# Kernel tuning notes

Measured on AMD Instinct MI355X. Metric: run time of the kernel, lower is better.

## Reference

```python
import jax, jax.numpy as jnp
import numpy as np

N, E, D = 50000, 500000, 128   # nodes, edges, input feature dim
H, F = 4, 32                    # num_heads, features_per_head (H*F == MLP output 128)


def _layer_norm(x, scale, bias, eps=1e-6):
    mu = jnp.mean(x, axis=-1, keepdims=True)
    var = jnp.var(x, axis=-1, keepdims=True)
    return (x - mu) * jax.lax.rsqrt(var + eps) * scale + bias


def setup_inputs() -> dict:
    key = jax.random.key(0)
    ks = jax.random.split(key, 6)
    s = lambda fan_in: 1.0 / np.sqrt(fan_in)
    return {
        "nodes": jax.random.normal(ks[0], (N, D), jnp.float32),
        "W1": jax.random.normal(ks[1], (D, 128), jnp.float32) * s(D),
        "b1": jnp.zeros((128,), jnp.float32),
        "ln1_scale": jnp.ones((128,), jnp.float32),
        "ln1_bias": jnp.zeros((128,), jnp.float32),
        "W2": jax.random.normal(ks[2], (128, H * F), jnp.float32) * s(128),
        "b2": jnp.zeros((H * F,), jnp.float32),
        "ln2_scale": jnp.ones((H * F,), jnp.float32),
        "ln2_bias": jnp.zeros((H * F,), jnp.float32),
        "senders": jax.random.randint(ks[3], (E,), 0, N, dtype=jnp.int32),
        "receivers": jax.random.randint(ks[4], (E,), 0, N, dtype=jnp.int32),
    }


def reference(nodes, W1, b1, ln1_scale, ln1_bias, W2, b2, ln2_scale, ln2_bias,
              senders, receivers):
    # attention_query MLP (MLPTorso: Dense -> LayerNorm -> relu, activate_final=True)
    h = jnp.maximum(_layer_norm(nodes @ W1 + b1, ln1_scale, ln1_bias), 0.0)
    h = jnp.maximum(_layer_norm(h @ W2 + b2, ln2_scale, ln2_bias), 0.0)
    q = h.reshape(N, H, F)                       # [N, H, F]

    # gather per-edge sender/receiver projections (same math as per-edge MLP)
    sent = q[senders]                            # [E, H, F]
    recv = q[receivers]                          # [E, H, F]

    # per-edge, per-head attention logits
    logits = jnp.einsum('ehf,ehf->eh', sent, recv) / jnp.sqrt(jnp.float32(F))

    # segment softmax over incoming edges of each receiver node (jraph semantics)
    seg_max = jax.ops.segment_max(logits, receivers, num_segments=N)
    seg_max = jnp.where(jnp.isfinite(seg_max), seg_max, 0.0)  # empty segments
    unnorm = jnp.exp(logits - seg_max[receivers])
    denom = jax.ops.segment_sum(unnorm, receivers, num_segments=N)
    weights = unnorm / denom[receivers]          # [E, H]

    # weighted messages, scatter-sum to receiver nodes
    messages = sent * weights[..., None]         # [E, H, F]
    agg = jax.ops.segment_sum(messages, receivers, num_segments=N)  # [N, H, F]

    # node update: activation then average over heads (avg_multi_head=True)
    out = jnp.maximum(agg, 0.0)
    return jnp.mean(out, axis=1)                 # [N, F]
```

## Files before the change

### kernel.cpp

```cpp
#include <hip/hip_runtime.h>

constexpr int D  = 128;
constexpr int NH = 4;
constexpr int NF = 32;

typedef __attribute__((ext_vector_type(8))) short bfrag;
typedef __attribute__((ext_vector_type(4))) float ffrag;

__device__ __forceinline__ unsigned short bf16h(float x) {
    unsigned u = __float_as_uint(x);
    u += 0x7fffu + ((u >> 16) & 1u);
    return (unsigned short)(u >> 16);
}
__device__ __forceinline__ float bf16tof(unsigned short h) {
    return __uint_as_float(((unsigned)h) << 16);
}

__global__ __launch_bounds__(256) void zero_cnt_kernel(int* __restrict__ p, int n)
{
    const int i4 = (blockIdx.x * blockDim.x + threadIdx.x) * 4;
    if (i4 + 3 < n) {
        *(int4*)&p[i4] = {0, 0, 0, 0};
    } else if (i4 < n) {
        for (int i = i4; i < n; ++i) p[i] = 0;
    }
}

__global__ __launch_bounds__(256) void wsplit_kernel(
    const float* __restrict__ W1, const float* __restrict__ W2,
    unsigned short* __restrict__ wt)
{
    const int L  = blockIdx.x >> 3;
    const int ct = blockIdx.x & 7;
    const float* W = L ? W2 : W1;
    const int ks   = threadIdx.x >> 6;
    const int lane = threadIdx.x & 63;
    const int lg = lane >> 4, lc = lane & 15;
    unsigned short* Hp = wt + ((size_t)(L * 2 + 0) * 32 + ct * 4 + ks) * 512 + lane * 8;
    unsigned short* Lp = wt + ((size_t)(L * 2 + 1) * 32 + ct * 4 + ks) * 512 + lane * 8;
    #pragma unroll
    for (int i = 0; i < 8; ++i) {
        const int k = ks * 32 + lg * 8 + i;
        const int c = ct * 16 + lc;
        const float v = W[(size_t)k * 128 + c];
        const unsigned short hh = bf16h(v);
        Hp[i] = hh;
        Lp[i] = bf16h(v - bf16tof(hh));
    }
}

__global__ __launch_bounds__(256, 2) void mlp_pipe_kernel(
    const float* __restrict__ X,
    const unsigned short* __restrict__ WF,
    const float* __restrict__ b1, const float* __restrict__ g1, const float* __restrict__ be1,
    const float* __restrict__ b2, const float* __restrict__ g2, const float* __restrict__ be2,
    unsigned short* __restrict__ Q, int N)
{
    constexpr int PW = 132;
    __shared__ unsigned HL[4 * 16 * PW];

    const int tid  = threadIdx.x;
    const int lane = tid & 63;
    const int wave = tid >> 6;
    const int lc   = lane & 15;
    const int lg   = lane >> 4;
    const int n0w  = (blockIdx.x * 4 + wave) * 16;
    if (n0w >= N) return;
    unsigned* hl = &HL[wave * 16 * PW];

    bfrag ah[4], al[4];

    {
        const int rowx = (n0w + lc < N) ? (n0w + lc) : (N - 1);
        const float* xr = X + (size_t)rowx * 128 + lg * 8;
        #pragma unroll
        for (int ks = 0; ks < 4; ++ks) {
            const float4 a = *(const float4*)&xr[ks * 32];
            const float4 b = *(const float4*)&xr[ks * 32 + 4];
            const float f[8] = {a.x, a.y, a.z, a.w, b.x, b.y, b.z, b.w};
            #pragma unroll
            for (int i = 0; i < 8; ++i) {
                const unsigned short hh = bf16h(f[i]);
                ah[ks][i] = (short)hh;
                al[ks][i] = (short)bf16h(f[i] - bf16tof(hh));
            }
        }
    }

    bfrag Bh0[4], Bl0[4], Bh1[4], Bl1[4];
    ffrag accF[8];

#define LOADB(BH, BL, hiBase, loBase, ctg)                                     \
    {                                                                          \
        const unsigned short* hp_ = WF + (size_t)((hiBase) + (ctg) * 4) * 512 + lane * 8; \
        const unsigned short* lp_ = WF + (size_t)((loBase) + (ctg) * 4) * 512 + lane * 8; \
        _Pragma("unroll")                                                      \
        for (int ks_ = 0; ks_ < 4; ++ks_) {                                    \
            BH[ks_] = *(const bfrag*)(hp_ + ks_ * 512);                        \
            BL[ks_] = *(const bfrag*)(lp_ + ks_ * 512);                        \
        }                                                                      \
    }

#define COMPB(BH, BL, dst)                                                     \
    {                                                                          \
        ffrag aH_ = (ffrag){0.f, 0.f, 0.f, 0.f};                               \
        ffrag aX_ = (ffrag){0.f, 0.f, 0.f, 0.f};                               \
        _Pragma("unroll")                                                      \
        for (int ks_ = 0; ks_ < 4; ++ks_) {                                    \
            aH_ = __builtin_amdgcn_mfma_f32_16x16x32_bf16(ah[ks_], BH[ks_], aH_, 0, 0, 0); \
            aX_ = __builtin_amdgcn_mfma_f32_16x16x32_bf16(ah[ks_], BL[ks_], aX_, 0, 0, 0); \
            aX_ = __builtin_amdgcn_mfma_f32_16x16x32_bf16(al[ks_], BH[ks_], aX_, 0, 0, 0); \
        }                                                                      \
        dst = aH_ + aX_;                                                       \
    }

#define GEMM_LAYER(hiBase, loBase)                                             \
    LOADB(Bh0, Bl0, hiBase, loBase, 0)                                         \
    LOADB(Bh1, Bl1, hiBase, loBase, 1)                                         \
    __builtin_amdgcn_sched_barrier(0);                                         \
    COMPB(Bh0, Bl0, accF[0])                                                   \
    LOADB(Bh0, Bl0, hiBase, loBase, 2)                                         \
    __builtin_amdgcn_sched_barrier(0);                                         \
    COMPB(Bh1, Bl1, accF[1])                                                   \
    LOADB(Bh1, Bl1, hiBase, loBase, 3)                                         \
    __builtin_amdgcn_sched_barrier(0);                                         \
    COMPB(Bh0, Bl0, accF[2])                                                   \
    LOADB(Bh0, Bl0, hiBase, loBase, 4)                                         \
    __builtin_amdgcn_sched_barrier(0);                                         \
    COMPB(Bh1, Bl1, accF[3])                                                   \
    LOADB(Bh1, Bl1, hiBase, loBase, 5)                                         \
    __builtin_amdgcn_sched_barrier(0);                                         \
    COMPB(Bh0, Bl0, accF[4])                                                   \
    LOADB(Bh0, Bl0, hiBase, loBase, 6)                                         \
    __builtin_amdgcn_sched_barrier(0);                                         \
    COMPB(Bh1, Bl1, accF[5])                                                   \
    LOADB(Bh1, Bl1, hiBase, loBase, 7)                                         \
    __builtin_amdgcn_sched_barrier(0);                                         \
    COMPB(Bh0, Bl0, accF[6])                                                   \
    COMPB(Bh1, Bl1, accF[7])

    GEMM_LAYER(0, 32)

    {
        float bb[8], gg[8], tt[8];
        #pragma unroll
        for (int ct = 0; ct < 8; ++ct) {
            const int col = ct * 16 + lc;
            bb[ct] = b1[col]; gg[ct] = g1[col]; tt[ct] = be1[col];
        }
        #pragma unroll
        for (int j = 0; j < 4; ++j) {
            float t[8], s = 0.f, ss = 0.f;
            #pragma unroll
            for (int ct = 0; ct < 8; ++ct) {
                t[ct] = accF[ct][j] + bb[ct];
                s += t[ct]; ss += t[ct] * t[ct];
            }
            #pragma unroll
            for (int off = 1; off <= 8; off <<= 1) {
                s  += __shfl_xor(s,  off, 16);
                ss += __shfl_xor(ss, off, 16);
            }
            const float mu   = s * (1.f / 128.f);
            const float var  = fmaxf(ss * (1.f / 128.f) - mu * mu, 0.f);
            const float rstd = rsqrtf(var + 1e-6f);
            const int row = lg * 4 + j;
            #pragma unroll
            for (int ct = 0; ct < 8; ++ct) {
                const float o = fmaxf((t[ct] - mu) * rstd * gg[ct] + tt[ct], 0.f);
                const unsigned short hh = bf16h(o);
                const unsigned short ll = bf16h(o - bf16tof(hh));
                hl[row * PW + ct * 16 + lc] = (unsigned)hh | ((unsigned)ll << 16);
            }
        }
    }

    asm volatile("s_waitcnt lgkmcnt(0)" ::: "memory");

    #pragma unroll
    for (int ks = 0; ks < 4; ++ks) {
        const uint4 r0 = *(const uint4*)&hl[lc * PW + ks * 32 + lg * 8];
        const uint4 r1 = *(const uint4*)&hl[lc * PW + ks * 32 + lg * 8 + 4];
        const unsigned rr[8] = {r0.x, r0.y, r0.z, r0.w, r1.x, r1.y, r1.z, r1.w};
        #pragma unroll
        for (int i = 0; i < 8; ++i) {
            ah[ks][i] = (short)(rr[i] & 0xffffu);
            al[ks][i] = (short)(rr[i] >> 16);
        }
    }

    GEMM_LAYER(64, 96)

#undef GEMM_LAYER
#undef COMPB
#undef LOADB

    {
        float bb[8], gg[8], tt[8];
        #pragma unroll
        for (int ct = 0; ct < 8; ++ct) {
            const int col = ct * 16 + lc;
            bb[ct] = b2[col]; gg[ct] = g2[col]; tt[ct] = be2[col];
        }
        #pragma unroll
        for (int j = 0; j < 4; ++j) {
            float t[8], s = 0.f, ss = 0.f;
            #pragma unroll
            for (int ct = 0; ct < 8; ++ct) {
                t[ct] = accF[ct][j] + bb[ct];
                s += t[ct]; ss += t[ct] * t[ct];
            }
            #pragma unroll
            for (int off = 1; off <= 8; off <<= 1) {
                s  += __shfl_xor(s,  off, 16);
                ss += __shfl_xor(ss, off, 16);
            }
            const float mu   = s * (1.f / 128.f);
            const float var  = fmaxf(ss * (1.f / 128.f) - mu * mu, 0.f);
            const float rstd = rsqrtf(var + 1e-6f);
            const int grow = n0w + lg * 4 + j;
            if (grow < N) {
                #pragma unroll
                for (int ct = 0; ct < 8; ++ct) {
                    const float o = fmaxf((t[ct] - mu) * rstd * gg[ct] + tt[ct], 0.f);
                    Q[(size_t)grow * 128 + ct * 16 + lc] = bf16h(o);
                }
            }
        }
    }
}

__global__ __launch_bounds__(256) void hist_kernel(
    const int* __restrict__ recv, int* __restrict__ cnt, int E)
{
    int i = blockIdx.x * blockDim.x + threadIdx.x;
    if (i < E) atomicAdd(&cnt[recv[i]], 1);
}

__global__ __launch_bounds__(256) void scan_blocks_kernel(
    const int* __restrict__ cnt, int* __restrict__ rowptr,
    int* __restrict__ bsum, int N)
{
    __shared__ int lds[256];
    const int tid = threadIdx.x;
    const int base = blockIdx.x * 1024 + tid * 4;
    int v0 = (base + 0 < N) ? cnt[base + 0] : 0;
    int v1 = (base + 1 < N) ? cnt[base + 1] : 0;
    int v2 = (base + 2 < N) ? cnt[base + 2] : 0;
    int v3 = (base + 3 < N) ? cnt[base + 3] : 0;
    const int tsum = v0 + v1 + v2 + v3;
    lds[tid] = tsum;
    __syncthreads();
    for (int off = 1; off < 256; off <<= 1) {
        int t = (tid >= off) ? lds[tid - off] : 0;
        __syncthreads();
        lds[tid] += t;
        __syncthreads();
    }
    int run = lds[tid] - tsum;
    if (base + 0 < N) rowptr[base + 0] = run;
    run += v0;
    if (base + 1 < N) rowptr[base + 1] = run;
    run += v1;
    if (base + 2 < N) rowptr[base + 2] = run;
    run += v2;
    if (base + 3 < N) rowptr[base + 3] = run;
    if (tid == 255) bsum[blockIdx.x] = lds[255];
}

__global__ __launch_bounds__(256) void scan_top_kernel(int* bsum, int nb)
{
    __shared__ int lds[256];
    const int tid = threadIdx.x;
    int v = (tid < nb) ? bsum[tid] : 0;
    lds[tid] = v;
    __syncthreads();
    for (int off = 1; off < 256; off <<= 1) {
        int t = (tid >= off) ? lds[tid - off] : 0;
        __syncthreads();
        lds[tid] += t;
        __syncthreads();
    }
    if (tid < nb) bsum[tid] = lds[tid] - v;
}

__global__ __launch_bounds__(256) void scan_add_kernel(
    int* __restrict__ rowptr, int* __restrict__ cursor,
    const int* __restrict__ bsum, int N, int E)
{
    int i = blockIdx.x * blockDim.x + threadIdx.x;
    if (i < N) {
        int v = rowptr[i] + bsum[i >> 10];
        rowptr[i] = v;
        cursor[i] = v;
    }
    if (i == 0) rowptr[N] = E;
}

__global__ __launch_bounds__(256) void fill_kernel(
    const int* __restrict__ senders, const int* __restrict__ receivers,
    int* __restrict__ cursor, int* __restrict__ ssend, int E)
{
    int e = blockIdx.x * blockDim.x + threadIdx.x;
    if (e < E) {
        int r = receivers[e];
        int pos = atomicAdd(&cursor[r], 1);
        ssend[pos] = senders[e];
    }
}

__global__ __launch_bounds__(256) void node_attn_kernel(
    const unsigned short* __restrict__ q, const int* __restrict__ rowptr,
    const int* __restrict__ ssend, float* __restrict__ out, int N)
{
    const int lane = threadIdx.x & 63;
    const int hl   = lane & 31;
    const int half = lane >> 5;
    const int wid  = (blockIdx.x * blockDim.x + threadIdx.x) >> 6;
    const int nw   = (gridDim.x * blockDim.x) >> 6;

    for (int n = wid; n < N; n += nw) {
        const uint2 braw = *(const uint2*)&q[(size_t)n * D + hl * 4];
        const float b0 = __uint_as_float(braw.x << 16);
        const float b1 = __uint_as_float(braw.x & 0xffff0000u);
        const float b2 = __uint_as_float(braw.y << 16);
        const float b3 = __uint_as_float(braw.y & 0xffff0000u);

        const int beg = rowptr[n], end = rowptr[n + 1];
        float m = -1e30f, l = 0.f;
        float c0 = 0.f, c1 = 0.f, c2 = 0.f, c3 = 0.f;

        int j = beg + half;
        uint2 raw = {0u, 0u};
        if (j < end)
            raw = *(const uint2*)&q[(size_t)ssend[j] * D + hl * 4];
        for (; j < end; j += 2) {
            const uint2 cur = raw;
            if (j + 2 < end)
                raw = *(const uint2*)&q[(size_t)ssend[j + 2] * D + hl * 4];
            const float a0 = __uint_as_float(cur.x << 16);
            const float a1 = __uint_as_float(cur.x & 0xffff0000u);
            const float a2 = __uint_as_float(cur.y << 16);
            const float a3 = __uint_as_float(cur.y & 0xffff0000u);
            float p = a0 * b0 + a1 * b1 + a2 * b2 + a3 * b3;
            p += __shfl_xor(p, 1);
            p += __shfl_xor(p, 2);
            p += __shfl_xor(p, 4);
            const float logit = p * 0.17677669529663687f;
            const float nm = fmaxf(m, logit);
            const float sc = __expf(m - nm);
            const float u  = __expf(logit - nm);
            l  = l * sc + u;
            c0 = c0 * sc + u * a0;
            c1 = c1 * sc + u * a1;
            c2 = c2 * sc + u * a2;
            c3 = c3 * sc + u * a3;
            m = nm;
        }

        const float om  = __shfl_xor(m, 32);
        const float ol  = __shfl_xor(l, 32);
        const float oc0 = __shfl_xor(c0, 32);
        const float oc1 = __shfl_xor(c1, 32);
        const float oc2 = __shfl_xor(c2, 32);
        const float oc3 = __shfl_xor(c3, 32);
        const float nm = fmaxf(m, om);
        const float s0 = __expf(m - nm), s1 = __expf(om - nm);
        const float lt = l * s0 + ol * s1;
        const float inv = (lt > 0.f) ? (1.f / lt) : 0.f;
        float r0 = fmaxf((c0 * s0 + oc0 * s1) * inv, 0.f);
        float r1 = fmaxf((c1 * s0 + oc1 * s1) * inv, 0.f);
        float r2 = fmaxf((c2 * s0 + oc2 * s1) * inv, 0.f);
        float r3 = fmaxf((c3 * s0 + oc3 * s1) * inv, 0.f);

        r0 += __shfl_xor(r0, 8);  r0 += __shfl_xor(r0, 16);
        r1 += __shfl_xor(r1, 8);  r1 += __shfl_xor(r1, 16);
        r2 += __shfl_xor(r2, 8);  r2 += __shfl_xor(r2, 16);
        r3 += __shfl_xor(r3, 8);  r3 += __shfl_xor(r3, 16);
        if (lane < 8) {
            float4 o = {0.25f * r0, 0.25f * r1, 0.25f * r2, 0.25f * r3};
            *(float4*)&out[(size_t)n * NF + lane * 4] = o;
        }
    }
}

extern "C" void kernel_launch(void* const* d_in, const int* in_sizes, int n_in,
                              void* d_out, int out_size, void* d_ws, size_t ws_size,
                              hipStream_t stream)
{
    const float* nodes = (const float*)d_in[0];
    const float* W1    = (const float*)d_in[1];
    const float* b1    = (const float*)d_in[2];
    const float* g1    = (const float*)d_in[3];
    const float* be1   = (const float*)d_in[4];
    const float* W2    = (const float*)d_in[5];
    const float* b2    = (const float*)d_in[6];
    const float* g2    = (const float*)d_in[7];
    const float* be2   = (const float*)d_in[8];
    const int* senders   = (const int*)d_in[9];
    const int* receivers = (const int*)d_in[10];

    const int N = in_sizes[0] / D;
    const int E = in_sizes[9];
    float* out = (float*)d_out;

    char* ws = (char*)d_ws;
    unsigned short* qb = (unsigned short*)ws; ws += (size_t)N * D * 2;
    unsigned short* wt = (unsigned short*)ws; ws += 4 * 128 * 128 * 2;
    int* cnt      = (int*)ws;    ws += (size_t)N * 4;
    int* rowptr   = (int*)ws;    ws += (size_t)(N + 2) * 4;
    int* cursor   = (int*)ws;    ws += (size_t)N * 4;
    int* bsum     = (int*)ws;    ws += 256 * 4;
    int* ssend    = (int*)ws;    ws += (size_t)E * 4;

    zero_cnt_kernel<<<(N / 4 + 255) / 256, 256, 0, stream>>>(cnt, N);

    wsplit_kernel<<<16, 256, 0, stream>>>(W1, W2, wt);
    const int nwt = (N + 15) / 16;
    mlp_pipe_kernel<<<(nwt + 3) / 4, 256, 0, stream>>>(
        nodes, wt, b1, g1, be1, b2, g2, be2, qb, N);

    const int nb = (N + 1023) / 1024;
    hist_kernel<<<(E + 255) / 256, 256, 0, stream>>>(receivers, cnt, E);
    scan_blocks_kernel<<<nb, 256, 0, stream>>>(cnt, rowptr, bsum, N);
    scan_top_kernel<<<1, 256, 0, stream>>>(bsum, nb);
    scan_add_kernel<<<(N + 255) / 256, 256, 0, stream>>>(rowptr, cursor, bsum, N, E);
    fill_kernel<<<(E + 255) / 256, 256, 0, stream>>>(senders, receivers, cursor, ssend, E);

    node_attn_kernel<<<(N + 3) / 4, 256, 0, stream>>>(qb, rowptr, ssend, out, N);
}
```

Before: 133.1 us.

## Merge prep kernels, fuse histogram into MLP launch, process two row tiles per wave

The weight split and count zeroing are merged into one prep kernel. The receiver histogram now runs in extra blocks of the MLP kernel, so the MLP and the atomic histogram overlap in one launch. Each MLP wave now handles 32 rows as two 16-row tiles that share the loaded B fragments, which halves weight loads per row and interleaves independent MFMA chains. The cost is more registers and twice the LDS per block, which may lower occupancy, and the histogram blocks compete for CUs with the MLP blocks.

```diff
diff --git a/kernel.cpp b/kernel.cpp
--- a/kernel.cpp
+++ b/kernel.cpp
@@ -16,62 +16,72 @@
     return __uint_as_float(((unsigned)h) << 16);
 }
 
-__global__ __launch_bounds__(256) void zero_cnt_kernel(int* __restrict__ p, int n)
-{
-    const int i4 = (blockIdx.x * blockDim.x + threadIdx.x) * 4;
-    if (i4 + 3 < n) {
-        *(int4*)&p[i4] = {0, 0, 0, 0};
-    } else if (i4 < n) {
-        for (int i = i4; i < n; ++i) p[i] = 0;
-    }
-}
-
-__global__ __launch_bounds__(256) void wsplit_kernel(
+__global__ __launch_bounds__(256) void prep_kernel(
     const float* __restrict__ W1, const float* __restrict__ W2,
-    unsigned short* __restrict__ wt)
-{
-    const int L  = blockIdx.x >> 3;
-    const int ct = blockIdx.x & 7;
-    const float* W = L ? W2 : W1;
-    const int ks   = threadIdx.x >> 6;
-    const int lane = threadIdx.x & 63;
-    const int lg = lane >> 4, lc = lane & 15;
-    unsigned short* Hp = wt + ((size_t)(L * 2 + 0) * 32 + ct * 4 + ks) * 512 + lane * 8;
-    unsigned short* Lp = wt + ((size_t)(L * 2 + 1) * 32 + ct * 4 + ks) * 512 + lane * 8;
-    #pragma unroll
-    for (int i = 0; i < 8; ++i) {
-        const int k = ks * 32 + lg * 8 + i;
-        const int c = ct * 16 + lc;
-        const float v = W[(size_t)k * 128 + c];
-        const unsigned short hh = bf16h(v);
-        Hp[i] = hh;
-        Lp[i] = bf16h(v - bf16tof(hh));
-    }
-}
-
-__global__ __launch_bounds__(256, 2) void mlp_pipe_kernel(
+    unsigned short* __restrict__ wt, int* __restrict__ cnt, int nz)
+{
+    if (blockIdx.x < 16) {
+        const int L  = blockIdx.x >> 3;
+        const int ct = blockIdx.x & 7;
+        const float* W = L ? W2 : W1;
+        const int ks   = threadIdx.x >> 6;
+        const int lane = threadIdx.x & 63;
+        const int lg = lane >> 4, lc = lane & 15;
+        unsigned short* Hp = wt + ((size_t)(L * 2 + 0) * 32 + ct * 4 + ks) * 512 + lane * 8;
+        unsigned short* Lp = wt + ((size_t)(L * 2 + 1) * 32 + ct * 4 + ks) * 512 + lane * 8;
+        #pragma unroll
+        for (int i = 0; i < 8; ++i) {
+            const int k = ks * 32 + lg * 8 + i;
+            const int c = ct * 16 + lc;
+            const float v = W[(size_t)k * 128 + c];
+            const unsigned short hh = bf16h(v);
+            Hp[i] = hh;
+            Lp[i] = bf16h(v - bf16tof(hh));
+        }
+    } else {
+        const int i4 = ((blockIdx.x - 16) * 256 + threadIdx.x) * 4;
+        if (i4 + 3 < nz) {
+            *(int4*)&cnt[i4] = {0, 0, 0, 0};
+        } else if (i4 < nz) {
+            for (int i = i4; i < nz; ++i) cnt[i] = 0;
+        }
+    }
+}
+
+__global__ __launch_bounds__(256, 2) void mlp_hist_kernel(
     const float* __restrict__ X,
     const unsigned short* __restrict__ WF,
     const float* __restrict__ b1, const float* __restrict__ g1, const float* __restrict__ be1,
     const float* __restrict__ b2, const float* __restrict__ g2, const float* __restrict__ be2,
-    unsigned short* __restrict__ Q, int N)
+    unsigned short* __restrict__ Q, int N,
+    const int* __restrict__ recv, int* __restrict__ cnt, int E, int mlpBlocks)
 {
     constexpr int PW = 132;
-    __shared__ unsigned HL[4 * 16 * PW];
+    __shared__ unsigned HL[4 * 2 * 16 * PW];
+
+    if (blockIdx.x >= mlpBlocks) {
+        const int tid0   = (blockIdx.x - mlpBlocks) * 256 + threadIdx.x;
+        const int stride = (gridDim.x - mlpBlocks) * 256;
+        for (int i = tid0; i < E; i += stride) atomicAdd(&cnt[recv[i]], 1);
+        return;
+    }
 
     const int tid  = threadIdx.x;
     const int lane = tid & 63;
     const int wave = tid >> 6;
     const int lc   = lane & 15;
     const int lg   = lane >> 4;
-    const int n0w  = (blockIdx.x * 4 + wave) * 16;
+    const int n0w  = (blockIdx.x * 4 + wave) * 32;
     if (n0w >= N) return;
-    unsigned* hl = &HL[wave * 16 * PW];
-
-    bfrag ah[4], al[4];
-
-    {
-        const int rowx = (n0w + lc < N) ? (n0w + lc) : (N - 1);
+    unsigned* hl0 = &HL[(wave * 2 + 0) * 16 * PW];
+    unsigned* hl1 = &HL[(wave * 2 + 1) * 16 * PW];
+
+    bfrag ah0[4], al0[4], ah1[4], al1[4];
+
+    #pragma unroll
+    for (int t = 0; t < 2; ++t) {
+        const int row = n0w + t * 16 + lc;
+        const int rowx = (row < N) ? row : (N - 1);
         const float* xr = X + (size_t)rowx * 128 + lg * 8;
         #pragma unroll
         for (int ks = 0; ks < 4; ++ks) {
@@ -81,14 +91,15 @@
             #pragma unroll
             for (int i = 0; i < 8; ++i) {
                 const unsigned short hh = bf16h(f[i]);
-                ah[ks][i] = (short)hh;
-                al[ks][i] = (short)bf16h(f[i] - bf16tof(hh));
+                const unsigned short ll = bf16h(f[i] - bf16tof(hh));
+                if (t == 0) { ah0[ks][i] = (short)hh; al0[ks][i] = (short)ll; }
+                else        { ah1[ks][i] = (short)hh; al1[ks][i] = (short)ll; }
             }
         }
     }
 
     bfrag Bh0[4], Bl0[4], Bh1[4], Bl1[4];
-    ffrag accF[8];
+    ffrag acc0[8], acc1[8];
 
 #define LOADB(BH, BL, hiBase, loBase, ctg)                                     \
     {                                                                          \
@@ -101,140 +112,150 @@
         }                                                                      \
     }
 
-#define COMPB(BH, BL, dst)                                                     \
+#define COMPB2(BH, BL, d0, d1)                                                 \
     {                                                                          \
-        ffrag aH_ = (ffrag){0.f, 0.f, 0.f, 0.f};                               \
-        ffrag aX_ = (ffrag){0.f, 0.f, 0.f, 0.f};                               \
+        ffrag aH0_ = (ffrag){0.f,0.f,0.f,0.f}, aX0_ = (ffrag){0.f,0.f,0.f,0.f};\
+        ffrag aH1_ = (ffrag){0.f,0.f,0.f,0.f}, aX1_ = (ffrag){0.f,0.f,0.f,0.f};\
         _Pragma("unroll")                                                      \
         for (int ks_ = 0; ks_ < 4; ++ks_) {                                    \
-            aH_ = __builtin_amdgcn_mfma_f32_16x16x32_bf16(ah[ks_], BH[ks_], aH_, 0, 0, 0); \
-            aX_ = __builtin_amdgcn_mfma_f32_16x16x32_bf16(ah[ks_], BL[ks_], aX_, 0, 0, 0); \
-            aX_ = __builtin_amdgcn_mfma_f32_16x16x32_bf16(al[ks_], BH[ks_], aX_, 0, 0, 0); \
+            aH0_ = __builtin_amdgcn_mfma_f32_16x16x32_bf16(ah0[ks_], BH[ks_], aH0_, 0, 0, 0); \
+            aH1_ = __builtin_amdgcn_mfma_f32_16x16x32_bf16(ah1[ks_], BH[ks_], aH1_, 0, 0, 0); \
+            aX0_ = __builtin_amdgcn_mfma_f32_16x16x32_bf16(ah0[ks_], BL[ks_], aX0_, 0, 0, 0); \
+            aX1_ = __builtin_amdgcn_mfma_f32_16x16x32_bf16(ah1[ks_], BL[ks_], aX1_, 0, 0, 0); \
+            aX0_ = __builtin_amdgcn_mfma_f32_16x16x32_bf16(al0[ks_], BH[ks_], aX0_, 0, 0, 0); \
+            aX1_ = __builtin_amdgcn_mfma_f32_16x16x32_bf16(al1[ks_], BH[ks_], aX1_, 0, 0, 0); \
         }                                                                      \
-        dst = aH_ + aX_;                                                       \
+        d0 = aH0_ + aX0_;                                                      \
+        d1 = aH1_ + aX1_;                                                      \
     }
 
 #define GEMM_LAYER(hiBase, loBase)                                             \
     LOADB(Bh0, Bl0, hiBase, loBase, 0)                                         \
     LOADB(Bh1, Bl1, hiBase, loBase, 1)                                         \
     __builtin_amdgcn_sched_barrier(0);                                         \
-    COMPB(Bh0, Bl0, accF[0])                                                   \
+    COMPB2(Bh0, Bl0, acc0[0], acc1[0])                                         \
     LOADB(Bh0, Bl0, hiBase, loBase, 2)                                         \
     __builtin_amdgcn_sched_barrier(0);                                         \
-    COMPB(Bh1, Bl1, accF[1])                                                   \
+    COMPB2(Bh1, Bl1, acc0[1], acc1[1])                                         \
     LOADB(Bh1, Bl1, hiBase, loBase, 3)                                         \
     __builtin_amdgcn_sched_barrier(0);                                         \
-    COMPB(Bh0, Bl0, accF[2])                                                   \
+    COMPB2(Bh0, Bl0, acc0[2], acc1[2])                                         \
     LOADB(Bh0, Bl0, hiBase, loBase, 4)                                         \
     __builtin_amdgcn_sched_barrier(0);                                         \
-    COMPB(Bh1, Bl1, accF[3])                                                   \
+    COMPB2(Bh1, Bl1, acc0[3], acc1[3])                                         \
     LOADB(Bh1, Bl1, hiBase, loBase, 5)                                         \
     __builtin_amdgcn_sched_barrier(0);                                         \
-    COMPB(Bh0, Bl0, accF[4])                                                   \
+    COMPB2(Bh0, Bl0, acc0[4], acc1[4])                                         \
     LOADB(Bh0, Bl0, hiBase, loBase, 6)                                         \
     __builtin_amdgcn_sched_barrier(0);                                         \
-    COMPB(Bh1, Bl1, accF[5])                                                   \
+    COMPB2(Bh1, Bl1, acc0[5], acc1[5])                                         \
     LOADB(Bh1, Bl1, hiBase, loBase, 7)                                         \
     __builtin_amdgcn_sched_barrier(0);                                         \
-    COMPB(Bh0, Bl0, accF[6])                                                   \
-    COMPB(Bh1, Bl1, accF[7])
+    COMPB2(Bh0, Bl0, acc0[6], acc1[6])                                         \
+    COMPB2(Bh1, Bl1, acc0[7], acc1[7])
+
+#define LN1_TILE(ACC, HLP)                                                     \
+    {                                                                          \
+        _Pragma("unroll")                                                      \
+        for (int j = 0; j < 4; ++j) {                                          \
+            float t_[8], s_ = 0.f, ss_ = 0.f;                                  \
+            _Pragma("unroll")                                                  \
+            for (int ct = 0; ct < 8; ++ct) {                                   \
+                t_[ct] = ACC[ct][j] + b1v[ct];                                 \
+                s_ += t_[ct]; ss_ += t_[ct] * t_[ct];                          \
+            }                                                                  \
+            _Pragma("unroll")                                                  \
+            for (int off = 1; off <= 8; off <<= 1) {                           \
+                s_  += __shfl_xor(s_,  off, 16);                               \
+                ss_ += __shfl_xor(ss_, off, 16);                               \
+            }                                                                  \
+            const float mu_   = s_ * (1.f / 128.f);                            \
+            const float var_  = fmaxf(ss_ * (1.f / 128.f) - mu_ * mu_, 0.f);   \
+            const float rstd_ = rsqrtf(var_ + 1e-6f);                          \
+            const int row_ = lg * 4 + j;                                       \
+            _Pragma("unroll")                                                  \
+            for (int ct = 0; ct < 8; ++ct) {                                   \
+                const float o_ = fmaxf((t_[ct] - mu_) * rstd_ * g1v[ct] + t1v[ct], 0.f); \
+                const unsigned short hh_ = bf16h(o_);                          \
+                const unsigned short ll_ = bf16h(o_ - bf16tof(hh_));           \
+                HLP[row_ * PW + ct * 16 + lc] = (unsigned)hh_ | ((unsigned)ll_ << 16); \
+            }                                                                  \
+        }                                                                      \
+    }
+
+#define LOADA2(AH, AL, HLP)                                                    \
+    _Pragma("unroll")                                                          \
+    for (int ks_ = 0; ks_ < 4; ++ks_) {                                        \
+        const uint4 r0_ = *(const uint4*)&HLP[lc * PW + ks_ * 32 + lg * 8];    \
+        const uint4 r1_ = *(const uint4*)&HLP[lc * PW + ks_ * 32 + lg * 8 + 4];\
+        const unsigned rr_[8] = {r0_.x, r0_.y, r0_.z, r0_.w,                   \
+                                 r1_.x, r1_.y, r1_.z, r1_.w};                  \
+        _Pragma("unroll")                                                      \
+        for (int i_ = 0; i_ < 8; ++i_) {                                       \
+            AH[ks_][i_] = (short)(rr_[i_] & 0xffffu);                          \
+            AL[ks_][i_] = (short)(rr_[i_] >> 16);                              \
+        }                                                                      \
+    }
+
+#define LN2_TILE(ACC, ROWBASE)                                                 \
+    {                                                                          \
+        _Pragma("unroll")                                                      \
+        for (int j = 0; j < 4; ++j) {                                          \
+            float t_[8], s_ = 0.f, ss_ = 0.f;                                  \
+            _Pragma("unroll")                                                  \
+            for (int ct = 0; ct < 8; ++ct) {                                   \
+                t_[ct] = ACC[ct][j] + b2v[ct];                                 \
+                s_ += t_[ct]; ss_ += t_[ct] * t_[ct];                          \
+            }                                                                  \
+            _Pragma("unroll")                                                  \
+            for (int off = 1; off <= 8; off <<= 1) {                           \
+                s_  += __shfl_xor(s_,  off, 16);                               \
+                ss_ += __shfl_xor(ss_, off, 16);                               \
+            }                                                                  \
+            const float mu_   = s_ * (1.f / 128.f);                            \
+            const float var_  = fmaxf(ss_ * (1.f / 128.f) - mu_ * mu_, 0.f);   \
+            const float rstd_ = rsqrtf(var_ + 1e-6f);                          \
+            const int grow_ = (ROWBASE) + lg * 4 + j;                          \
+            if (grow_ < N) {                                                   \
+                _Pragma("unroll")                                              \
+                for (int ct = 0; ct < 8; ++ct) {                               \
+                    const float o_ = fmaxf((t_[ct] - mu_) * rstd_ * g2v[ct] + t2v[ct], 0.f); \
+                    Q[(size_t)grow_ * 128 + ct * 16 + lc] = bf16h(o_);         \
+                }                                                              \
+            }                                                                  \
+        }                                                                      \
+    }
+
+    float b1v[8], g1v[8], t1v[8], b2v[8], g2v[8], t2v[8];
+    #pragma unroll
+    for (int ct = 0; ct < 8; ++ct) {
+        const int col = ct * 16 + lc;
+        b1v[ct] = b1[col]; g1v[ct] = g1[col]; t1v[ct] = be1[col];
+        b2v[ct] = b2[col]; g2v[ct] = g2[col]; t2v[ct] = be2[col];
+    }
 
     GEMM_LAYER(0, 32)
 
-    {
-        float bb[8], gg[8], tt[8];
-        #pragma unroll
-        for (int ct = 0; ct < 8; ++ct) {
-            const int col = ct * 16 + lc;
-            bb[ct] = b1[col]; gg[ct] = g1[col]; tt[ct] = be1[col];
-        }
-        #pragma unroll
-        for (int j = 0; j < 4; ++j) {
-            float t[8], s = 0.f, ss = 0.f;
-            #pragma unroll
-            for (int ct = 0; ct < 8; ++ct) {
-                t[ct] = accF[ct][j] + bb[ct];
-                s += t[ct]; ss += t[ct] * t[ct];
-            }
-            #pragma unroll
-            for (int off = 1; off <= 8; off <<= 1) {
-                s  += __shfl_xor(s,  off, 16);
-                ss += __shfl_xor(ss, off, 16);
-            }
-            const float mu   = s * (1.f / 128.f);
-            const float var  = fmaxf(ss * (1.f / 128.f) - mu * mu, 0.f);
-            const float rstd = rsqrtf(var + 1e-6f);
-            const int row = lg * 4 + j;
-            #pragma unroll
-            for (int ct = 0; ct < 8; ++ct) {
-                const float o = fmaxf((t[ct] - mu) * rstd * gg[ct] + tt[ct], 0.f);
-                const unsigned short hh = bf16h(o);
-                const unsigned short ll = bf16h(o - bf16tof(hh));
-                hl[row * PW + ct * 16 + lc] = (unsigned)hh | ((unsigned)ll << 16);
-            }
-        }
-    }
+    LN1_TILE(acc0, hl0)
+    LN1_TILE(acc1, hl1)
 
     asm volatile("s_waitcnt lgkmcnt(0)" ::: "memory");
-
-    #pragma unroll
-    for (int ks = 0; ks < 4; ++ks) {
-        const uint4 r0 = *(const uint4*)&hl[lc * PW + ks * 32 + lg * 8];
-        const uint4 r1 = *(const uint4*)&hl[lc * PW + ks * 32 + lg * 8 + 4];
-        const unsigned rr[8] = {r0.x, r0.y, r0.z, r0.w, r1.x, r1.y, r1.z, r1.w};
-        #pragma unroll
-        for (int i = 0; i < 8; ++i) {
-            ah[ks][i] = (short)(rr[i] & 0xffffu);
-            al[ks][i] = (short)(rr[i] >> 16);
-        }
-    }
+    __builtin_amdgcn_sched_barrier(0);
+
+    LOADA2(ah0, al0, hl0)
+    LOADA2(ah1, al1, hl1)
 
     GEMM_LAYER(64, 96)
 
+    LN2_TILE(acc0, n0w)
+    LN2_TILE(acc1, n0w + 16)
+
+#undef LN2_TILE
+#undef LOADA2
+#undef LN1_TILE
 #undef GEMM_LAYER
-#undef COMPB
+#undef COMPB2
 #undef LOADB
-
-    {
-        float bb[8], gg[8], tt[8];
-        #pragma unroll
-        for (int ct = 0; ct < 8; ++ct) {
-            const int col = ct * 16 + lc;
-            bb[ct] = b2[col]; gg[ct] = g2[col]; tt[ct] = be2[col];
-        }
-        #pragma unroll
-        for (int j = 0; j < 4; ++j) {
-            float t[8], s = 0.f, ss = 0.f;
-            #pragma unroll
-            for (int ct = 0; ct < 8; ++ct) {
-                t[ct] = accF[ct][j] + bb[ct];
-                s += t[ct]; ss += t[ct] * t[ct];
-            }
-            #pragma unroll
-            for (int off = 1; off <= 8; off <<= 1) {
-                s  += __shfl_xor(s,  off, 16);
-                ss += __shfl_xor(ss, off, 16);
-            }
-            const float mu   = s * (1.f / 128.f);
-            const float var  = fmaxf(ss * (1.f / 128.f) - mu * mu, 0.f);
-            const float rstd = rsqrtf(var + 1e-6f);
-            const int grow = n0w + lg * 4 + j;
-            if (grow < N) {
-                #pragma unroll
-                for (int ct = 0; ct < 8; ++ct) {
-                    const float o = fmaxf((t[ct] - mu) * rstd * gg[ct] + tt[ct], 0.f);
-                    Q[(size_t)grow * 128 + ct * 16 + lc] = bf16h(o);
-                }
-            }
-        }
-    }
-}
-
-__global__ __launch_bounds__(256) void hist_kernel(
-    const int* __restrict__ recv, int* __restrict__ cnt, int E)
-{
-    int i = blockIdx.x * blockDim.x + threadIdx.x;
-    if (i < E) atomicAdd(&cnt[recv[i]], 1);
 }
 
 __global__ __launch_bounds__(256) void scan_blocks_kernel(
@@ -413,18 +434,21 @@
     int* bsum     = (int*)ws;    ws += 256 * 4;
     int* ssend    = (int*)ws;    ws += (size_t)E * 4;
 
-    zero_cnt_kernel<<<(N / 4 + 255) / 256, 256, 0, stream>>>(cnt, N);
-
-    wsplit_kernel<<<16, 256, 0, stream>>>(W1, W2, wt);
-    const int nwt = (N + 15) / 16;
-    mlp_pipe_kernel<<<(nwt + 3) / 4, 256, 0, stream>>>(
-        nodes, wt, b1, g1, be1, b2, g2, be2, qb, N);
-
+    const int zb = (N + 1023) / 1024;
+    const int nwt32 = (N + 31) / 32;
+    const int mlpBlocks = (nwt32 + 3) / 4;
     const int nb = (N + 1023) / 1024;
-    hist_kernel<<<(E + 255) / 256, 256, 0, stream>>>(receivers, cnt, E);
+
+    prep_kernel<<<16 + zb, 256, 0, stream>>>(W1, W2, wt, cnt, N);
+
+    mlp_hist_kernel<<<mlpBlocks + 128, 256, 0, stream>>>(
+        nodes, wt, b1, g1, be1, b2, g2, be2, qb, N,
+        receivers, cnt, E, mlpBlocks);
+
     scan_blocks_kernel<<<nb, 256, 0, stream>>>(cnt, rowptr, bsum, N);
     scan_top_kernel<<<1, 256, 0, stream>>>(bsum, nb);
     scan_add_kernel<<<(N + 255) / 256, 256, 0, stream>>>(rowptr, cursor, bsum, N, E);
+
     fill_kernel<<<(E + 255) / 256, 256, 0, stream>>>(senders, receivers, cursor, ssend, E);
 
     node_attn_kernel<<<(N + 3) / 4, 256, 0, stream>>>(qb, rowptr, ssend, out, N);
```

After: 116.3 us. 1.14x faster.
